# Performance work log

Hardware: AMD Instinct MI355X
Metric: run time of the kernel (lower is better)

The kernel has to match this reference:

```python
import jax, jax.numpy as jnp
import numpy as np

N = 20000
E = 640000
R = 8          # num_rels == num_bases (basis regularizer with num_bases=-1)
B = 8
IN_SIZE = 128
HID = 256      # 4 * fea_dimen
FEA = 64
TIME = 2880
POI = 12


def setup_inputs() -> dict:
    key = jax.random.key(0)
    ks = jax.random.split(key, 20)
    s = 0.02
    inp = {
        'src': jax.random.randint(ks[0], (E,), 0, N),
        'dst': jax.random.randint(ks[1], (E,), 0, N),
        'etype': jax.random.randint(ks[2], (E,), 0, R),
        'poi_distribution': jax.random.normal(ks[3], (N, POI), jnp.float32),
        'time_distribution': jax.random.normal(ks[4], (N, TIME), jnp.float32),
        'road_feature': jax.random.normal(ks[5], (N, IN_SIZE), jnp.float32),
        # input projections
        'poi_w': jax.random.normal(ks[6], (POI, FEA), jnp.float32) * s,
        'poi_b': jnp.zeros((FEA,), jnp.float32),
        'time_w': jax.random.normal(ks[7], (TIME, 2 * FEA), jnp.float32) * s,
        'time_b': jnp.zeros((2 * FEA,), jnp.float32),
        'road_w': jax.random.normal(ks[8], (IN_SIZE, FEA), jnp.float32) * s,
        'road_b': jnp.zeros((FEA,), jnp.float32),
        # RelGraphConv layer 1 (basis decomposition)
        'basis1': jax.random.normal(ks[9], (B, HID, HID), jnp.float32) * s,
        'coef1': jax.random.normal(ks[10], (R, B), jnp.float32) * s,
        'loop_w1': jax.random.normal(ks[11], (HID, HID), jnp.float32) * s,
        'bias1': jnp.zeros((HID,), jnp.float32),
        # RelGraphConv layer 2
        'basis2': jax.random.normal(ks[12], (B, HID, HID), jnp.float32) * s,
        'coef2': jax.random.normal(ks[13], (R, B), jnp.float32) * s,
        'loop_w2': jax.random.normal(ks[14], (HID, HID), jnp.float32) * s,
        'bias2': jnp.zeros((HID,), jnp.float32),
    }
    return inp


def _rel_graph_conv(h, src, dst, etype, basis, coef, loop_w, bias):
    # W_r = sum_b coef[r,b] * basis[b]  -> (R, HID, HID), small
    W = jnp.einsum('rb,bio->rio', coef, basis)
    # transform every node by every relation weight, then gather per edge
    y = jnp.einsum('ni,rio->nro', h, W)          # (N, R, HID)
    msgs = y[src, etype]                          # (E, HID) gather
    agg = jax.ops.segment_sum(msgs, dst, num_segments=h.shape[0])  # scatter-sum
    return agg + h @ loop_w + bias


def reference(src, dst, etype, poi_distribution, time_distribution, road_feature,
              poi_w, poi_b, time_w, time_b, road_w, road_b,
              basis1, coef1, loop_w1, bias1, basis2, coef2, loop_w2, bias2):
    poi_feat = poi_distribution @ poi_w + poi_b       # (N, 64)
    time_feat = time_distribution @ time_w + time_b   # (N, 128)
    road_feat = road_feature @ road_w + road_b        # (N, 64)
    feat = jnp.concatenate([poi_feat, time_feat, road_feat], axis=1)  # (N, 256)
    h = _rel_graph_conv(feat, src, dst, etype, basis1, coef1, loop_w1, bias1)
    h = jax.nn.relu(h)  # dropout=0.0 -> identity
    h = _rel_graph_conv(h, src, dst, etype, basis2, coef2, loop_w2, bias2)
    return h
```

## Files before the change

kernel.cpp:

```cpp
#include <hip/hip_runtime.h>

#define NN 20000
#define NE 640000
#define NR 8
#define NB 8
#define HID 256
#define KPOI 12
#define KTIME 2880
#define KROAD 128
#define NK (NN * NR)
#define SPLITK 5
#define KCH (KTIME / SPLITK)

typedef __attribute__((ext_vector_type(8))) short bf8_t;
typedef __attribute__((ext_vector_type(4))) float f4_t;

__device__ inline unsigned short f2bf(float f) {
  unsigned int u = __float_as_uint(f);
  u += 0x7FFF + ((u >> 16) & 1);
  return (unsigned short)(u >> 16);
}
__device__ inline float bf2f(unsigned short h) {
  return __uint_as_float((unsigned int)h << 16);
}

__global__ __launch_bounds__(256) void make_WT12(
    const float* __restrict__ coef1, const float* __restrict__ basis1,
    const float* __restrict__ coef2, const float* __restrict__ basis2,
    unsigned short* __restrict__ WT) {
  int idx = blockIdx.x * 256 + threadIdx.x;
  int r = idx >> 16;
  int o = (idx >> 8) & 255;
  int i = idx & 255;
  const float* coef  = (r < NR) ? coef1 : coef2;
  const float* basis = (r < NR) ? basis1 : basis2;
  int rr = r & 7;
  float acc = 0.f;
#pragma unroll
  for (int b = 0; b < NB; ++b)
    acc += coef[rr * NB + b] * basis[b * HID * HID + i * HID + o];
  WT[idx] = f2bf(acc);
}

__global__ __launch_bounds__(256) void transp_LW(
    const float* __restrict__ w1, const float* __restrict__ w2,
    unsigned short* __restrict__ L1, unsigned short* __restrict__ L2) {
  int idx = blockIdx.x * 256 + threadIdx.x;
  int sel = idx >> 16;
  int j = idx & 65535;
  int r = j >> 8, c = j & 255;
  const float* in = sel ? w2 : w1;
  unsigned short* out = sel ? L2 : L1;
  out[c * HID + r] = f2bf(in[j]);
}

__global__ __launch_bounds__(256) void transp_bf16(const float* __restrict__ in,
                                                   unsigned short* __restrict__ out,
                                                   int R, int Cc) {
  int idx = blockIdx.x * 256 + threadIdx.x;
  if (idx >= R * Cc) return;
  int r = idx / Cc, c = idx - r * Cc;
  out[(size_t)c * R + r] = f2bf(in[idx]);
}

#define BK 16
template<int BM, int BN, int TM, int TN>
__global__ __launch_bounds__(256) void sgemm_bf(
    int M, int Nn, int K,
    const float* __restrict__ A, int lda,
    const float* __restrict__ B, int ldb,
    const float* __restrict__ bias,
    unsigned short* __restrict__ C, int ldc)
{
  constexpr int SA = BM + 4;
  constexpr int SB = BN + 4;
  __shared__ float As[BK * SA];
  __shared__ float Bs[BK * SB];
  const int tid = threadIdx.x;
  const int brow = blockIdx.x * BM;
  const int bcol = blockIdx.y * BN;
  constexpr int TCOLS = BN / TN;
  const int row0 = (tid / TCOLS) * TM;
  const int col0 = (tid % TCOLS) * TN;

  float acc[TM][TN] = {};

  for (int kb = 0; kb < K; kb += BK) {
    constexpr int AIT = (BM * 4) / 256;
#pragma unroll
    for (int it = 0; it < AIT; ++it) {
      int i = tid + it * 256;
      int r = i >> 2, q = (i & 3) * 4;
      int grow = brow + r, gk = kb + q;
      if (grow < M && gk + 3 < K) {
        float4 v = *(const float4*)(A + (size_t)grow * lda + gk);
        As[(q + 0) * SA + r] = v.x;
        As[(q + 1) * SA + r] = v.y;
        As[(q + 2) * SA + r] = v.z;
        As[(q + 3) * SA + r] = v.w;
      } else {
#pragma unroll
        for (int j = 0; j < 4; ++j)
          As[(q + j) * SA + r] =
              (grow < M && gk + j < K) ? A[(size_t)grow * lda + gk + j] : 0.f;
      }
    }
    constexpr int BIT = (BN * 4) / 256;
#pragma unroll
    for (int it = 0; it < BIT; ++it) {
      int i = tid + it * 256;
      int k = i / (BN / 4), cq = (i % (BN / 4)) * 4;
      int gk = kb + k, gc = bcol + cq;
      float4 v = {0.f, 0.f, 0.f, 0.f};
      if (gk < K) {
        if (gc + 3 < Nn) {
          v = *(const float4*)(B + (size_t)gk * ldb + gc);
        } else {
#pragma unroll
          for (int j = 0; j < 4; ++j)
            if (gc + j < Nn) (&v.x)[j] = B[(size_t)gk * ldb + gc + j];
        }
      }
      *(float4*)(&Bs[k * SB + cq]) = v;
    }
    __syncthreads();
#pragma unroll
    for (int kk = 0; kk < BK; ++kk) {
      float a[TM], b[TN];
#pragma unroll
      for (int i = 0; i < TM; i += 4)
        *(float4*)(&a[i]) = *(const float4*)(&As[kk * SA + row0 + i]);
#pragma unroll
      for (int j = 0; j < TN; j += 4)
        *(float4*)(&b[j]) = *(const float4*)(&Bs[kk * SB + col0 + j]);
#pragma unroll
      for (int i = 0; i < TM; ++i)
#pragma unroll
        for (int j = 0; j < TN; ++j)
          acc[i][j] += a[i] * b[j];
    }
    __syncthreads();
  }

  float bcache[TN];
#pragma unroll
  for (int j = 0; j < TN; ++j)
    bcache[j] = bias ? bias[bcol + col0 + j] : 0.f;
#pragma unroll
  for (int i = 0; i < TM; ++i) {
    int row = brow + row0 + i;
    if (row >= M) continue;
#pragma unroll
    for (int j = 0; j < TN; ++j) {
      int col = bcol + col0 + j;
      if (col < Nn)
        C[(size_t)row * ldc + col] = f2bf(acc[i][j] + bcache[j]);
    }
  }
}

__global__ __launch_bounds__(256) void mfma_time_sk(
    const float* __restrict__ A,
    const unsigned short* __restrict__ BT,
    float* __restrict__ TP)
{
  __shared__ __align__(16) char ldsA[32 * 128];
  __shared__ __align__(16) char ldsB[128 * 128];
  const int tid = threadIdx.x;
  const int lane = tid & 63;
  const int w = tid >> 6;
  const int brow = blockIdx.x * 32;
  const int kb0 = blockIdx.y * KCH;

  f4_t acc[2][2];
#pragma unroll
  for (int i = 0; i < 2; ++i)
#pragma unroll
    for (int j = 0; j < 2; ++j) acc[i][j] = (f4_t){0.f, 0.f, 0.f, 0.f};

  for (int kb = kb0; kb < kb0 + KCH; kb += 64) {
    {
      int r = tid >> 3, c8 = tid & 7;
      const float* ap = A + (size_t)(brow + r) * KTIME + kb + c8 * 8;
      f4_t v0 = *(const f4_t*)ap;
      f4_t v1 = *(const f4_t*)(ap + 4);
      unsigned short hh[8];
#pragma unroll
      for (int j = 0; j < 4; ++j) { hh[j] = f2bf(v0[j]); hh[4 + j] = f2bf(v1[j]); }
      *(bf8_t*)(ldsA + r * 128 + ((c8 * 16) ^ ((r & 7) << 4))) = *(bf8_t*)hh;
    }
#pragma unroll
    for (int it = 0; it < 4; ++it) {
      int slot = tid + it * 256;
      int r = slot >> 3, c8 = slot & 7;
      bf8_t v = *(const bf8_t*)(BT + (size_t)r * KTIME + kb + c8 * 8);
      *(bf8_t*)(ldsB + r * 128 + ((c8 * 16) ^ ((r & 7) << 4))) = v;
    }
    __syncthreads();
#pragma unroll
    for (int ks = 0; ks < 2; ++ks) {
      const int kbyte = ks * 64 + (lane >> 4) * 16;
      bf8_t af[2], bfr[2];
#pragma unroll
      for (int mi = 0; mi < 2; ++mi) {
        int m = mi * 16 + (lane & 15);
        af[mi] = *(const bf8_t*)(ldsA + m * 128 + (kbyte ^ ((m & 7) << 4)));
      }
#pragma unroll
      for (int ni = 0; ni < 2; ++ni) {
        int n = w * 32 + ni * 16 + (lane & 15);
        bfr[ni] = *(const bf8_t*)(ldsB + n * 128 + (kbyte ^ ((n & 7) << 4)));
      }
#pragma unroll
      for (int mi = 0; mi < 2; ++mi)
#pragma unroll
        for (int ni = 0; ni < 2; ++ni)
          acc[mi][ni] = __builtin_amdgcn_mfma_f32_16x16x32_bf16(
              af[mi], bfr[ni], acc[mi][ni], 0, 0, 0);
    }
    __syncthreads();
  }

  float* tp = TP + (size_t)blockIdx.y * NN * 128;
  const int rq = (lane >> 4) * 4;
  const int cl = lane & 15;
#pragma unroll
  for (int ni = 0; ni < 2; ++ni) {
    int c = w * 32 + ni * 16 + cl;
#pragma unroll
    for (int mi = 0; mi < 2; ++mi) {
#pragma unroll
      for (int j = 0; j < 4; ++j) {
        int row = brow + mi * 16 + rq + j;
        tp[(size_t)row * 128 + c] = acc[mi][ni][j];
      }
    }
  }
}

__global__ __launch_bounds__(256) void time_finish(
    const float* __restrict__ TP, const float* __restrict__ bias,
    unsigned short* __restrict__ featb) {
  int i = blockIdx.x * 256 + threadIdx.x;
  if (i >= NN * 32) return;
  int row = i >> 5, c4 = (i & 31) * 4;
  f4_t s = *(const f4_t*)(TP + (size_t)row * 128 + c4);
#pragma unroll
  for (int k = 1; k < SPLITK; ++k) {
    f4_t v = *(const f4_t*)(TP + (size_t)k * NN * 128 + (size_t)row * 128 + c4);
    s.x += v.x; s.y += v.y; s.z += v.z; s.w += v.w;
  }
  f4_t b = *(const f4_t*)(bias + c4);
  unsigned short h[4] = {f2bf(s.x + b.x), f2bf(s.y + b.y),
                         f2bf(s.z + b.z), f2bf(s.w + b.w)};
  *(ushort4*)(featb + (size_t)row * 256 + 64 + c4) = *(ushort4*)h;
}

__global__ __launch_bounds__(256) void agg_k(
    const int* __restrict__ offs, const unsigned short* __restrict__ ssrc,
    const unsigned short* __restrict__ hin, unsigned short* __restrict__ Z) {
  int w = (blockIdx.x * 256 + threadIdx.x) >> 6;
  int lane = threadIdx.x & 63;
  if (w >= NR * NN) return;
  int q = w / NN;
  int d = w - q * NN;
  int lo = offs[d * NR + q];
  int hi = offs[d * NR + q + 1];
  f4_t az = {0.f, 0.f, 0.f, 0.f};
  int e = lo;
  for (; e + 4 <= hi; e += 4) {
    int s0 = ssrc[e], s1 = ssrc[e + 1], s2 = ssrc[e + 2], s3 = ssrc[e + 3];
    ushort4 u0 = *(const ushort4*)(hin + (size_t)s0 * HID + lane * 4);
    ushort4 u1 = *(const ushort4*)(hin + (size_t)s1 * HID + lane * 4);
    ushort4 u2 = *(const ushort4*)(hin + (size_t)s2 * HID + lane * 4);
    ushort4 u3 = *(const ushort4*)(hin + (size_t)s3 * HID + lane * 4);
    az.x += (bf2f(u0.x) + bf2f(u1.x)) + (bf2f(u2.x) + bf2f(u3.x));
    az.y += (bf2f(u0.y) + bf2f(u1.y)) + (bf2f(u2.y) + bf2f(u3.y));
    az.z += (bf2f(u0.z) + bf2f(u1.z)) + (bf2f(u2.z) + bf2f(u3.z));
    az.w += (bf2f(u0.w) + bf2f(u1.w)) + (bf2f(u2.w) + bf2f(u3.w));
  }
  for (; e < hi; ++e) {
    int s = ssrc[e];
    ushort4 u = *(const ushort4*)(hin + (size_t)s * HID + lane * 4);
    az.x += bf2f(u.x); az.y += bf2f(u.y);
    az.z += bf2f(u.z); az.w += bf2f(u.w);
  }
  unsigned short hz[4] = {f2bf(az.x), f2bf(az.y), f2bf(az.z), f2bf(az.w)};
  *(ushort4*)(Z + (size_t)w * HID + lane * 4) = *(ushort4*)hz;
}

template<int EPI>
__global__ __launch_bounds__(512) void gemm_acc(
    const unsigned short* __restrict__ hbufA,
    const unsigned short* __restrict__ Z,
    const unsigned short* __restrict__ WT,
    const unsigned short* __restrict__ LWT,
    const float* __restrict__ bias,
    float* __restrict__ C, unsigned short* __restrict__ hb)
{
  __shared__ __align__(16) char At[32 * 512];
  __shared__ __align__(16) char Bt[256 * 128];
  const int tid = threadIdx.x;
  const int lane = tid & 63;
  const int w = tid >> 6;
  const int wr = w >> 2;
  const int wc = w & 3;
  const int brow = blockIdx.x * 32;

  f4_t acc[4];
#pragma unroll
  for (int i = 0; i < 4; ++i) acc[i] = (f4_t){0.f, 0.f, 0.f, 0.f};

#pragma unroll 1
  for (int s = 0; s < NR + 1; ++s) {
    const unsigned short* Asrc = (s == 0) ? hbufA : Z + (size_t)(s - 1) * NN * HID;
    const unsigned short* Wsrc = (s == 0) ? LWT : WT + (size_t)(s - 1) * HID * HID;
#pragma unroll
    for (int it = 0; it < 2; ++it) {
      int slot = tid + it * 512;
      int r = slot >> 5, c16 = slot & 31;
      bf8_t v = *(const bf8_t*)(Asrc + (size_t)(brow + r) * HID + c16 * 8);
      *(bf8_t*)(At + r * 512 + ((c16 * 16) ^ ((r & 7) << 4))) = v;
    }
    __syncthreads();
#pragma unroll 1
    for (int kc = 0; kc < 4; ++kc) {
#pragma unroll
      for (int it = 0; it < 4; ++it) {
        int slot = tid + it * 512;
        int n = slot >> 3, c8 = slot & 7;
        bf8_t v = *(const bf8_t*)(Wsrc + (size_t)n * HID + kc * 64 + c8 * 8);
        *(bf8_t*)(Bt + n * 128 + ((c8 * 16) ^ ((n & 7) << 4))) = v;
      }
      __syncthreads();
#pragma unroll
      for (int ks = 0; ks < 2; ++ks) {
        const int kbyte = ks * 64 + (lane >> 4) * 16;
        int m = wr * 16 + (lane & 15);
        bf8_t af = *(const bf8_t*)(
            At + m * 512 + ((kc * 128 + kbyte) ^ ((m & 7) << 4)));
#pragma unroll
        for (int ni = 0; ni < 4; ++ni) {
          int n = wc * 64 + ni * 16 + (lane & 15);
          bf8_t bfr = *(const bf8_t*)(Bt + n * 128 + (kbyte ^ ((n & 7) << 4)));
          acc[ni] = __builtin_amdgcn_mfma_f32_16x16x32_bf16(af, bfr, acc[ni], 0, 0, 0);
        }
      }
      __syncthreads();
    }
  }

  const int rq = (lane >> 4) * 4;
  const int cl = lane & 15;
#pragma unroll
  for (int ni = 0; ni < 4; ++ni) {
    int c = wc * 64 + ni * 16 + cl;
    float bv = bias[c];
#pragma unroll
    for (int j = 0; j < 4; ++j) {
      int row = brow + wr * 16 + rq + j;
      size_t o = (size_t)row * 256 + c;
      float v = acc[ni][j] + bv;
      if (EPI == 0) C[o] = v;
      else          hb[o] = f2bf(fmaxf(v, 0.f));
    }
  }
}

__global__ __launch_bounds__(256) void hist_k(const int* __restrict__ dst,
                                              const int* __restrict__ et,
                                              int* __restrict__ counts) {
  int e = blockIdx.x * 256 + threadIdx.x;
  if (e < NE) atomicAdd(&counts[dst[e] * NR + et[e]], 1);
}

__global__ __launch_bounds__(256) void scan_block(const int* __restrict__ counts,
                                                  int* __restrict__ offs,
                                                  int* __restrict__ bsums) {
  __shared__ int sh[256];
  int base = blockIdx.x * 1024;
  int t = threadIdx.x;
  int v[4];
  int s = 0;
#pragma unroll
  for (int j = 0; j < 4; ++j) {
    int idx = base + t * 4 + j;
    v[j] = (idx < NK) ? counts[idx] : 0;
    s += v[j];
  }
  sh[t] = s;
  __syncthreads();
  for (int off = 1; off < 256; off <<= 1) {
    int x = (t >= off) ? sh[t - off] : 0;
    __syncthreads();
    sh[t] += x;
    __syncthreads();
  }
  int run = sh[t] - s;
#pragma unroll
  for (int j = 0; j < 4; ++j) {
    int idx = base + t * 4 + j;
    if (idx < NK) offs[idx] = run;
    run += v[j];
  }
  if (t == 255) bsums[blockIdx.x] = sh[255];
}

__global__ __launch_bounds__(256) void scan_bsums(int* __restrict__ bsums, int nblk) {
  __shared__ int sh[256];
  int t = threadIdx.x;
  int own = (t < nblk) ? bsums[t] : 0;
  sh[t] = own;
  __syncthreads();
  for (int off = 1; off < 256; off <<= 1) {
    int x = (t >= off) ? sh[t - off] : 0;
    __syncthreads();
    sh[t] += x;
    __syncthreads();
  }
  int ex = sh[t] - own;
  if (t < nblk) bsums[t] = ex;
}

__global__ __launch_bounds__(256) void add_base(int* __restrict__ offs,
                                                const int* __restrict__ bsums,
                                                int* __restrict__ cursor) {
  int idx = blockIdx.x * 256 + threadIdx.x;
  if (idx < NK) {
    int v = offs[idx] + bsums[idx >> 10];
    offs[idx] = v;
    cursor[idx] = v;
  }
  if (idx == NK) offs[NK] = NE;
}

__global__ __launch_bounds__(256) void fill_k(const int* __restrict__ src,
                                              const int* __restrict__ dst,
                                              const int* __restrict__ et,
                                              int* __restrict__ cursor,
                                              unsigned short* __restrict__ ssrc) {
  int e = blockIdx.x * 256 + threadIdx.x;
  if (e < NE) {
    int key = dst[e] * NR + et[e];
    int p = atomicAdd(&cursor[key], 1);
    ssrc[p] = (unsigned short)src[e];
  }
}

extern "C" void kernel_launch(void* const* d_in, const int* in_sizes, int n_in,
                              void* d_out, int out_size, void* d_ws, size_t ws_size,
                              hipStream_t stream) {
  const int*   srcp      = (const int*)d_in[0];
  const int*   dstp      = (const int*)d_in[1];
  const int*   etypep    = (const int*)d_in[2];
  const float* poi_dist  = (const float*)d_in[3];
  const float* time_dist = (const float*)d_in[4];
  const float* road_feat = (const float*)d_in[5];
  const float* poi_w     = (const float*)d_in[6];
  const float* poi_b     = (const float*)d_in[7];
  const float* time_w    = (const float*)d_in[8];
  const float* time_b    = (const float*)d_in[9];
  const float* road_w    = (const float*)d_in[10];
  const float* road_b    = (const float*)d_in[11];
  const float* basis1    = (const float*)d_in[12];
  const float* coef1     = (const float*)d_in[13];
  const float* loop_w1   = (const float*)d_in[14];
  const float* bias1     = (const float*)d_in[15];
  const float* basis2    = (const float*)d_in[16];
  const float* coef2     = (const float*)d_in[17];
  const float* loop_w2   = (const float*)d_in[18];
  const float* bias2     = (const float*)d_in[19];

  float* out = (float*)d_out;

  char* ws = (char*)d_ws;
  unsigned short* WT1    = (unsigned short*)(ws);
  unsigned short* WT2    = (unsigned short*)(ws + 1048576);
  unsigned short* LWT1   = (unsigned short*)(ws + 2097152);
  unsigned short* LWT2   = (unsigned short*)(ws + 2228224);
  unsigned short* TWT    = (unsigned short*)(ws + 2359296);
  unsigned short* hbuf   = (unsigned short*)(ws + 3096576);
  unsigned short* Z      = (unsigned short*)(ws + 13336576);
  float*          TP     = (float*)(ws + 95256576);
  int*            offs   = (int*)  (ws + 146456576);
  int*            bsums  = (int*)  (ws + 147096592);
  unsigned short* ssrc   = (unsigned short*)(ws + 147097616);
  int*            counts = (int*)Z;
  int*            cursor = (int*)TP;

  dim3 blk(256);
  const int MG64 = (NN + 63) / 64;

  hipMemsetAsync(counts, 0, NK * sizeof(int), stream);
  hist_k<<<NE / 256, blk, 0, stream>>>(dstp, etypep, counts);
  scan_block<<<(NK + 1023) / 1024, blk, 0, stream>>>(counts, offs, bsums);
  scan_bsums<<<1, blk, 0, stream>>>(bsums, (NK + 1023) / 1024);
  add_base<<<(NK + 1 + 255) / 256, blk, 0, stream>>>(offs, bsums, cursor);
  fill_k<<<NE / 256, blk, 0, stream>>>(srcp, dstp, etypep, cursor, ssrc);

  transp_LW<<<2 * HID * HID / 256, blk, 0, stream>>>(loop_w1, loop_w2, LWT1, LWT2);
  transp_bf16<<<(KTIME * 128 + 255) / 256, blk, 0, stream>>>(time_w, TWT, KTIME, 128);
  make_WT12<<<2 * NR * HID * HID / 256, blk, 0, stream>>>(coef1, basis1,
                                                          coef2, basis2, WT1);

  sgemm_bf<64, 64, 4, 4><<<dim3(MG64, 1), blk, 0, stream>>>(
      NN, 64, KPOI, poi_dist, KPOI, poi_w, 64, poi_b, hbuf + 0, HID);
  mfma_time_sk<<<dim3(NN / 32, SPLITK), blk, 0, stream>>>(time_dist, TWT, TP);
  time_finish<<<(NN * 32 + 255) / 256, blk, 0, stream>>>(TP, time_b, hbuf);
  sgemm_bf<64, 64, 4, 4><<<dim3(MG64, 1), blk, 0, stream>>>(
      NN, 64, KROAD, road_feat, KROAD, road_w, 64, road_b, hbuf + 192, HID);

  agg_k<<<(NR * NN) / 4, blk, 0, stream>>>(offs, ssrc, hbuf, Z);
  gemm_acc<2><<<NN / 32, 512, 0, stream>>>(hbuf, Z, WT1, LWT1, bias1,
                                           nullptr, hbuf);

  agg_k<<<(NR * NN) / 4, blk, 0, stream>>>(offs, ssrc, hbuf, Z);
  gemm_acc<0><<<NN / 32, 512, 0, stream>>>(hbuf, Z, WT2, LWT2, bias2,
                                           out, nullptr);
}
```

Before: 461.6 us.

## Transform-then-gather RGCN: per-relation GEMM to Y, then fused gather-sum epilogue

Swaps the aggregate-then-transform order. Each layer now runs one GEMM that multiplies every node by all 8 relation weights plus the self-loop weight into a bf16 Y buffer, followed by a gather kernel that sums Y rows per destination over the CSR, adding bias, self-loop and ReLU. The 8 per-relation Z partial sums and their write/read round trip go away, and the weight build now uses a tiled LDS transpose for coalesced stores. In exchange, Y needs 9×N×HID of workspace, the edge gathers now read relation-specific Y slices instead of one shared h, and per-edge messages are rounded to bf16 before they are summed.

```diff
diff --git a/kernel.cpp b/kernel.cpp
--- a/kernel.cpp
+++ b/kernel.cpp
@@ -24,22 +24,40 @@
   return __uint_as_float((unsigned int)h << 16);
 }
 
-__global__ __launch_bounds__(256) void make_WT12(
+__global__ __launch_bounds__(256) void make_WT_t(
     const float* __restrict__ coef1, const float* __restrict__ basis1,
     const float* __restrict__ coef2, const float* __restrict__ basis2,
     unsigned short* __restrict__ WT) {
-  int idx = blockIdx.x * 256 + threadIdx.x;
-  int r = idx >> 16;
-  int o = (idx >> 8) & 255;
-  int i = idx & 255;
-  const float* coef  = (r < NR) ? coef1 : coef2;
-  const float* basis = (r < NR) ? basis1 : basis2;
-  int rr = r & 7;
-  float acc = 0.f;
-#pragma unroll
-  for (int b = 0; b < NB; ++b)
-    acc += coef[rr * NB + b] * basis[b * HID * HID + i * HID + o];
-  WT[idx] = f2bf(acc);
+  __shared__ unsigned short T[64][66];
+  const int bid = blockIdx.x;
+  const int lr = bid >> 4;
+  const int it = (bid >> 2) & 3, ot = bid & 3;
+  const int i0 = it * 64, o0 = ot * 64;
+  const float* coef  = (lr < NR) ? coef1 : coef2;
+  const float* basis = (lr < NR) ? basis1 : basis2;
+  const int r = lr & 7;
+  float cf[NB];
+#pragma unroll
+  for (int b = 0; b < NB; ++b) cf[b] = coef[r * NB + b];
+  const int to = threadIdx.x & 63;
+  const int tq = threadIdx.x >> 6;
+#pragma unroll
+  for (int k = 0; k < 16; ++k) {
+    int i_loc = tq * 16 + k;
+    int i = i0 + i_loc;
+    float acc = 0.f;
+#pragma unroll
+    for (int b = 0; b < NB; ++b)
+      acc += cf[b] * basis[((size_t)(b * HID + i)) * HID + o0 + to];
+    T[i_loc][to] = f2bf(acc);
+  }
+  __syncthreads();
+#pragma unroll
+  for (int k = 0; k < 16; ++k) {
+    int o_loc = tq * 16 + k;
+    WT[(size_t)lr * HID * HID + (size_t)(o0 + o_loc) * HID + i0 + to] =
+        T[to][o_loc];
+  }
 }
 
 __global__ __launch_bounds__(256) void transp_LW(
@@ -256,73 +274,41 @@
   *(ushort4*)(featb + (size_t)row * 256 + 64 + c4) = *(ushort4*)h;
 }
 
-__global__ __launch_bounds__(256) void agg_k(
-    const int* __restrict__ offs, const unsigned short* __restrict__ ssrc,
-    const unsigned short* __restrict__ hin, unsigned short* __restrict__ Z) {
-  int w = (blockIdx.x * 256 + threadIdx.x) >> 6;
-  int lane = threadIdx.x & 63;
-  if (w >= NR * NN) return;
-  int q = w / NN;
-  int d = w - q * NN;
-  int lo = offs[d * NR + q];
-  int hi = offs[d * NR + q + 1];
-  f4_t az = {0.f, 0.f, 0.f, 0.f};
-  int e = lo;
-  for (; e + 4 <= hi; e += 4) {
-    int s0 = ssrc[e], s1 = ssrc[e + 1], s2 = ssrc[e + 2], s3 = ssrc[e + 3];
-    ushort4 u0 = *(const ushort4*)(hin + (size_t)s0 * HID + lane * 4);
-    ushort4 u1 = *(const ushort4*)(hin + (size_t)s1 * HID + lane * 4);
-    ushort4 u2 = *(const ushort4*)(hin + (size_t)s2 * HID + lane * 4);
-    ushort4 u3 = *(const ushort4*)(hin + (size_t)s3 * HID + lane * 4);
-    az.x += (bf2f(u0.x) + bf2f(u1.x)) + (bf2f(u2.x) + bf2f(u3.x));
-    az.y += (bf2f(u0.y) + bf2f(u1.y)) + (bf2f(u2.y) + bf2f(u3.y));
-    az.z += (bf2f(u0.z) + bf2f(u1.z)) + (bf2f(u2.z) + bf2f(u3.z));
-    az.w += (bf2f(u0.w) + bf2f(u1.w)) + (bf2f(u2.w) + bf2f(u3.w));
-  }
-  for (; e < hi; ++e) {
-    int s = ssrc[e];
-    ushort4 u = *(const ushort4*)(hin + (size_t)s * HID + lane * 4);
-    az.x += bf2f(u.x); az.y += bf2f(u.y);
-    az.z += bf2f(u.z); az.w += bf2f(u.w);
-  }
-  unsigned short hz[4] = {f2bf(az.x), f2bf(az.y), f2bf(az.z), f2bf(az.w)};
-  *(ushort4*)(Z + (size_t)w * HID + lane * 4) = *(ushort4*)hz;
-}
-
-template<int EPI>
-__global__ __launch_bounds__(512) void gemm_acc(
-    const unsigned short* __restrict__ hbufA,
-    const unsigned short* __restrict__ Z,
+__global__ __launch_bounds__(512) void gemm_y(
+    const unsigned short* __restrict__ hin,
     const unsigned short* __restrict__ WT,
     const unsigned short* __restrict__ LWT,
-    const float* __restrict__ bias,
-    float* __restrict__ C, unsigned short* __restrict__ hb)
+    unsigned short* __restrict__ Y)
 {
-  __shared__ __align__(16) char At[32 * 512];
+  __shared__ __align__(16) char At[64 * 512];
   __shared__ __align__(16) char Bt[256 * 128];
   const int tid = threadIdx.x;
   const int lane = tid & 63;
   const int w = tid >> 6;
-  const int wr = w >> 2;
-  const int wc = w & 3;
-  const int brow = blockIdx.x * 32;
-
-  f4_t acc[4];
-#pragma unroll
-  for (int i = 0; i < 4; ++i) acc[i] = (f4_t){0.f, 0.f, 0.f, 0.f};
+  const int wr = w >> 1;
+  const int wc = w & 1;
+  const int brow = blockIdx.x * 64;
+
+#pragma unroll
+  for (int it = 0; it < 4; ++it) {
+    int slot = tid + it * 512;
+    int r = slot >> 5, c16 = slot & 31;
+    bf8_t v = {0, 0, 0, 0, 0, 0, 0, 0};
+    int grow = brow + r;
+    if (grow < NN) v = *(const bf8_t*)(hin + (size_t)grow * HID + c16 * 8);
+    *(bf8_t*)(At + r * 512 + ((c16 * 16) ^ ((r & 7) << 4))) = v;
+  }
+  __syncthreads();
+
+  const int rq = (lane >> 4) * 4;
+  const int cl = lane & 15;
 
 #pragma unroll 1
   for (int s = 0; s < NR + 1; ++s) {
-    const unsigned short* Asrc = (s == 0) ? hbufA : Z + (size_t)(s - 1) * NN * HID;
-    const unsigned short* Wsrc = (s == 0) ? LWT : WT + (size_t)(s - 1) * HID * HID;
-#pragma unroll
-    for (int it = 0; it < 2; ++it) {
-      int slot = tid + it * 512;
-      int r = slot >> 5, c16 = slot & 31;
-      bf8_t v = *(const bf8_t*)(Asrc + (size_t)(brow + r) * HID + c16 * 8);
-      *(bf8_t*)(At + r * 512 + ((c16 * 16) ^ ((r & 7) << 4))) = v;
-    }
-    __syncthreads();
+    const unsigned short* Wsrc = (s < NR) ? (WT + (size_t)s * HID * HID) : LWT;
+    f4_t acc[8];
+#pragma unroll
+    for (int i = 0; i < 8; ++i) acc[i] = (f4_t){0.f, 0.f, 0.f, 0.f};
 #pragma unroll 1
     for (int kc = 0; kc < 4; ++kc) {
 #pragma unroll
@@ -340,30 +326,74 @@
         bf8_t af = *(const bf8_t*)(
             At + m * 512 + ((kc * 128 + kbyte) ^ ((m & 7) << 4)));
 #pragma unroll
-        for (int ni = 0; ni < 4; ++ni) {
-          int n = wc * 64 + ni * 16 + (lane & 15);
+        for (int ni = 0; ni < 8; ++ni) {
+          int n = wc * 128 + ni * 16 + (lane & 15);
           bf8_t bfr = *(const bf8_t*)(Bt + n * 128 + (kbyte ^ ((n & 7) << 4)));
           acc[ni] = __builtin_amdgcn_mfma_f32_16x16x32_bf16(af, bfr, acc[ni], 0, 0, 0);
         }
       }
       __syncthreads();
     }
-  }
-
-  const int rq = (lane >> 4) * 4;
-  const int cl = lane & 15;
-#pragma unroll
-  for (int ni = 0; ni < 4; ++ni) {
-    int c = wc * 64 + ni * 16 + cl;
-    float bv = bias[c];
-#pragma unroll
-    for (int j = 0; j < 4; ++j) {
-      int row = brow + wr * 16 + rq + j;
-      size_t o = (size_t)row * 256 + c;
-      float v = acc[ni][j] + bv;
-      if (EPI == 0) C[o] = v;
-      else          hb[o] = f2bf(fmaxf(v, 0.f));
-    }
+    unsigned short* Ys = Y + (size_t)s * NN * HID;
+#pragma unroll
+    for (int ni = 0; ni < 8; ++ni) {
+      int c = wc * 128 + ni * 16 + cl;
+#pragma unroll
+      for (int j = 0; j < 4; ++j) {
+        int row = brow + wr * 16 + rq + j;
+        if (row < NN) Ys[(size_t)row * HID + c] = f2bf(acc[ni][j]);
+      }
+    }
+  }
+}
+
+template<int EPI>
+__global__ __launch_bounds__(256) void gather_k(
+    const int* __restrict__ offs, const unsigned short* __restrict__ ssrc,
+    const unsigned short* __restrict__ Y,
+    const float* __restrict__ bias,
+    unsigned short* __restrict__ hb, float* __restrict__ C)
+{
+  int d = (blockIdx.x * 256 + threadIdx.x) >> 6;
+  int lane = threadIdx.x & 63;
+  if (d >= NN) return;
+  const size_t SL = (size_t)NN * HID;
+
+  f4_t acc = *(const f4_t*)(bias + lane * 4);
+  {
+    ushort4 u = *(const ushort4*)(Y + (size_t)NR * SL + (size_t)d * HID + lane * 4);
+    acc.x += bf2f(u.x); acc.y += bf2f(u.y);
+    acc.z += bf2f(u.z); acc.w += bf2f(u.w);
+  }
+  int o[NR + 1];
+#pragma unroll
+  for (int r = 0; r <= NR; ++r) o[r] = offs[d * NR + r];
+#pragma unroll 1
+  for (int r = 0; r < NR; ++r) {
+    const unsigned short* Yr = Y + (size_t)r * SL;
+    int e = o[r], hi = o[r + 1];
+    for (; e + 2 <= hi; e += 2) {
+      int s0 = ssrc[e], s1 = ssrc[e + 1];
+      ushort4 u0 = *(const ushort4*)(Yr + (size_t)s0 * HID + lane * 4);
+      ushort4 u1 = *(const ushort4*)(Yr + (size_t)s1 * HID + lane * 4);
+      acc.x += bf2f(u0.x) + bf2f(u1.x);
+      acc.y += bf2f(u0.y) + bf2f(u1.y);
+      acc.z += bf2f(u0.z) + bf2f(u1.z);
+      acc.w += bf2f(u0.w) + bf2f(u1.w);
+    }
+    if (e < hi) {
+      int s = ssrc[e];
+      ushort4 u = *(const ushort4*)(Yr + (size_t)s * HID + lane * 4);
+      acc.x += bf2f(u.x); acc.y += bf2f(u.y);
+      acc.z += bf2f(u.z); acc.w += bf2f(u.w);
+    }
+  }
+  if (EPI == 1) {
+    unsigned short h[4] = {f2bf(fmaxf(acc.x, 0.f)), f2bf(fmaxf(acc.y, 0.f)),
+                           f2bf(fmaxf(acc.z, 0.f)), f2bf(fmaxf(acc.w, 0.f))};
+    *(ushort4*)(hb + (size_t)d * HID + lane * 4) = *(ushort4*)h;
+  } else {
+    *(f4_t*)(C + (size_t)d * HID + lane * 4) = acc;
   }
 }
 
@@ -474,19 +504,21 @@
   float* out = (float*)d_out;
 
   char* ws = (char*)d_ws;
-  unsigned short* WT1    = (unsigned short*)(ws);
-  unsigned short* WT2    = (unsigned short*)(ws + 1048576);
+  unsigned short* WT12   = (unsigned short*)(ws);
   unsigned short* LWT1   = (unsigned short*)(ws + 2097152);
   unsigned short* LWT2   = (unsigned short*)(ws + 2228224);
   unsigned short* TWT    = (unsigned short*)(ws + 2359296);
   unsigned short* hbuf   = (unsigned short*)(ws + 3096576);
-  unsigned short* Z      = (unsigned short*)(ws + 13336576);
-  float*          TP     = (float*)(ws + 95256576);
-  int*            offs   = (int*)  (ws + 146456576);
-  int*            bsums  = (int*)  (ws + 147096592);
-  unsigned short* ssrc   = (unsigned short*)(ws + 147097616);
-  int*            counts = (int*)Z;
+  unsigned short* Y      = (unsigned short*)(ws + 13336576);
+  float*          TP     = (float*)(ws + 105496576);
+  int*            offs   = (int*)  (ws + 156696576);
+  int*            bsums  = (int*)  (ws + 157336592);
+  unsigned short* ssrc   = (unsigned short*)(ws + 157337616);
+  int*            counts = (int*)Y;
   int*            cursor = (int*)TP;
+
+  unsigned short* WT1 = WT12;
+  unsigned short* WT2 = WT12 + (size_t)NR * HID * HID;
 
   dim3 blk(256);
   const int MG64 = (NN + 63) / 64;
@@ -500,8 +532,7 @@
 
   transp_LW<<<2 * HID * HID / 256, blk, 0, stream>>>(loop_w1, loop_w2, LWT1, LWT2);
   transp_bf16<<<(KTIME * 128 + 255) / 256, blk, 0, stream>>>(time_w, TWT, KTIME, 128);
-  make_WT12<<<2 * NR * HID * HID / 256, blk, 0, stream>>>(coef1, basis1,
-                                                          coef2, basis2, WT1);
+  make_WT_t<<<2 * NR * 16, blk, 0, stream>>>(coef1, basis1, coef2, basis2, WT12);
 
   sgemm_bf<64, 64, 4, 4><<<dim3(MG64, 1), blk, 0, stream>>>(
       NN, 64, KPOI, poi_dist, KPOI, poi_w, 64, poi_b, hbuf + 0, HID);
@@ -510,11 +541,9 @@
   sgemm_bf<64, 64, 4, 4><<<dim3(MG64, 1), blk, 0, stream>>>(
       NN, 64, KROAD, road_feat, KROAD, road_w, 64, road_b, hbuf + 192, HID);
 
-  agg_k<<<(NR * NN) / 4, blk, 0, stream>>>(offs, ssrc, hbuf, Z);
-  gemm_acc<2><<<NN / 32, 512, 0, stream>>>(hbuf, Z, WT1, LWT1, bias1,
-                                           nullptr, hbuf);
-
-  agg_k<<<(NR * NN) / 4, blk, 0, stream>>>(offs, ssrc, hbuf, Z);
-  gemm_acc<0><<<NN / 32, 512, 0, stream>>>(hbuf, Z, WT2, LWT2, bias2,
-                                           out, nullptr);
-}
+  gemm_y<<<MG64, 512, 0, stream>>>(hbuf, WT1, LWT1, Y);
+  gather_k<1><<<(NN + 3) / 4, blk, 0, stream>>>(offs, ssrc, Y, bias1, hbuf, nullptr);
+
+  gemm_y<<<MG64, 512, 0, stream>>>(hbuf, WT2, LWT2, Y);
+  gather_k<0><<<(NN + 3) / 4, blk, 0, stream>>>(offs, ssrc, Y, bias2, nullptr, out);
+}
```

Result: slower. 474.8 us (+2.9%).
